# Performance work log

Hardware: AMD Instinct MI355X
Metric: run time of the kernel (lower is better)

Reference implementation:

```python
import jax, jax.numpy as jnp
import numpy as np

N = 50000   # nodes
E = 800000  # edges (before self-loops)
IN = 256    # in_dim
H = 4       # heads
C = 64      # out_dim per head
NEG_SLOPE = 0.2
BN_EPS = 1e-5


def setup_inputs() -> dict:
    key = jax.random.key(0)
    ks = jax.random.split(key, 6)
    feature = jax.random.normal(ks[0], (N, IN), jnp.float32)
    edge_index = jax.random.randint(ks[1], (2, E), 0, N, dtype=jnp.int64)
    W = jax.random.normal(ks[2], (IN, H * C), jnp.float32) * 0.05
    att_src = jax.random.normal(ks[3], (H, C), jnp.float32) * 0.1
    att_dst = jax.random.normal(ks[4], (H, C), jnp.float32) * 0.1
    bias = jnp.zeros((H * C,), jnp.float32)
    gamma = jnp.ones((H * C,), jnp.float32)
    beta = jnp.zeros((H * C,), jnp.float32)
    return {"feature": feature, "edge_index": edge_index, "W": W,
            "att_src": att_src, "att_dst": att_dst, "bias": bias,
            "gamma": gamma, "beta": beta}


def reference(feature, edge_index, W, att_src, att_dst, bias, gamma, beta):
    n = feature.shape[0]
    # linear projection -> [N, H, C]
    x = (feature @ W).reshape(n, H, C)
    # per-node attention logits [N, H]
    a_src = jnp.einsum('nhc,hc->nh', x, att_src)
    a_dst = jnp.einsum('nhc,hc->nh', x, att_dst)
    # add self loops (PyG GATConv default)
    loop = jnp.arange(n, dtype=edge_index.dtype)
    src = jnp.concatenate([edge_index[0], loop])
    dst = jnp.concatenate([edge_index[1], loop])
    # edge attention scores [E+N, H]
    e = jax.nn.leaky_relu(a_src[src] + a_dst[dst], NEG_SLOPE)
    # segment softmax over incoming edges of each dst node
    m = jax.ops.segment_max(e, dst, num_segments=n)
    ex = jnp.exp(e - m[dst])
    denom = jax.ops.segment_sum(ex, dst, num_segments=n)
    alpha = ex / denom[dst]                       # [E+N, H]
    # weighted message aggregation -> [N, H, C]
    msg = x[src] * alpha[:, :, None]
    out = jax.ops.segment_sum(msg, dst, num_segments=n)
    h = out.reshape(n, H * C) + bias
    # batchnorm over nodes (training-mode batch statistics)
    mu = jnp.mean(h, axis=0)
    var = jnp.var(h, axis=0)
    h = (h - mu) * jax.lax.rsqrt(var + BN_EPS) * gamma + beta
    # ELU activation
    h = jax.nn.elu(h)
    # residual (in_dim == out_dim * num_heads)
    return feature + h
```

## Files before the change

kernel.cpp:

```cpp
#include <hip/hip_runtime.h>

#define N_NODES 50000
#define N_EDGES 800000
#define NEG_SLOPE 0.2f
#define BN_EPS  1e-5f
#define LOG2E   1.44269504088896f

#define CHUNKS 256
#define EDGES_PER_CHUNK 3125
#define NCOARSE 1024
#define NBUCKET 782

typedef short bf16x8 __attribute__((ext_vector_type(8)));
typedef float floatx4 __attribute__((ext_vector_type(4)));

__device__ inline ushort f2bf(float f) {
    union { float f; unsigned u; } v; v.f = f;
    unsigned r = v.u + 0x7fff + ((v.u >> 16) & 1);
    return (ushort)(r >> 16);
}
__device__ inline float bf2f(ushort h) {
    union { unsigned u; float f; } v; v.u = ((unsigned)h) << 16;
    return v.f;
}

__global__ __launch_bounds__(256) void count_wt_kernel(const int* __restrict__ ei,
                                                       const float* __restrict__ W,
                                                       int* __restrict__ counts,
                                                       ushort* __restrict__ Wtb,
                                                       float* __restrict__ gsum,
                                                       float* __restrict__ gsumsq)
{
    __shared__ int hist[NCOARSE];
    const int t = threadIdx.x;
    const int b = blockIdx.x;
    if (b < CHUNKS) {
        for (int j = t; j < NCOARSE; j += 256) hist[j] = 0;
        __syncthreads();
        const int e0 = b * EDGES_PER_CHUNK;
        for (int e = e0 + t; e < e0 + EDGES_PER_CHUNK; e += 256)
            atomicAdd(&hist[ei[N_EDGES + e] >> 6], 1);
        __syncthreads();
        for (int j = t; j < NCOARSE; j += 256)
            counts[j * CHUNKS + b] = hist[j];
    } else {
        const int n = b - CHUNKS;
        Wtb[n * 256 + t] = f2bf(W[t * 256 + n]);
        if (n == 0) { gsum[t] = 0.f; gsumsq[t] = 0.f; }
    }
}

__global__ __launch_bounds__(256) void sscan1_kernel(int* __restrict__ counts,
                                                     int* __restrict__ blocksum)
{
    __shared__ int sm[256];
    const int t = threadIdx.x;
    const int i = blockIdx.x * 256 + t;
    const int v = counts[i];
    sm[t] = v;
    __syncthreads();
#pragma unroll
    for (int off = 1; off < 256; off <<= 1) {
        const int u = (t >= off) ? sm[t - off] : 0;
        __syncthreads();
        sm[t] += u;
        __syncthreads();
    }
    counts[i] = sm[t] - v;
    if (t == 255) blocksum[blockIdx.x] = sm[255];
}

__global__ __launch_bounds__(256) void bucket_scatter_kernel(const int* __restrict__ ei,
                                                             const int* __restrict__ counts,
                                                             const int* __restrict__ blocksum,
                                                             int* __restrict__ blockbase,
                                                             uint* __restrict__ tmp)
{
    __shared__ int sm[256];
    __shared__ int bbase[NCOARSE];
    __shared__ int cursor[NCOARSE];
    const int t = threadIdx.x;
    const int blk = blockIdx.x;

    int v[4], loc[4], tot = 0;
#pragma unroll
    for (int j = 0; j < 4; ++j) {
        v[j] = blocksum[t * 4 + j];
        loc[j] = tot;
        tot += v[j];
    }
    sm[t] = tot;
    __syncthreads();
#pragma unroll
    for (int off = 1; off < 256; off <<= 1) {
        const int u = (t >= off) ? sm[t - off] : 0;
        __syncthreads();
        sm[t] += u;
        __syncthreads();
    }
    const int base = sm[t] - tot;
#pragma unroll
    for (int j = 0; j < 4; ++j) bbase[t * 4 + j] = base + loc[j];
    if (blk == 0) {
#pragma unroll
        for (int j = 0; j < 4; ++j) blockbase[t * 4 + j] = base + loc[j];
    }
    __syncthreads();

    for (int u = t; u < NCOARSE; u += 256)
        cursor[u] = counts[u * CHUNKS + blk] + bbase[u];
    __syncthreads();
    const int e0 = blk * EDGES_PER_CHUNK;
    for (int e = e0 + t; e < e0 + EDGES_PER_CHUNK; e += 256) {
        const int src = ei[e];
        const int dst = ei[N_EDGES + e];
        const int pos = atomicAdd(&cursor[dst >> 6], 1);
        tmp[pos] = ((uint)src << 6) | (uint)(dst & 63);
    }
}

__global__ __launch_bounds__(256) void bucket_build_kernel(const uint* __restrict__ tmp,
                                                           const int* __restrict__ blockbase,
                                                           int* __restrict__ offsets,
                                                           int* __restrict__ csr_src)
{
    __shared__ int hist[64];
    __shared__ int sbuf[64];
    __shared__ int cursor[64];
    const int t = threadIdx.x;
    const int b = blockIdx.x;
    const int start = blockbase[b];
    const int end   = blockbase[b + 1];
    if (t < 64) hist[t] = 0;
    __syncthreads();
    for (int e = start + t; e < end; e += 256)
        atomicAdd(&hist[tmp[e] & 63], 1);
    __syncthreads();
    const int v = (t < 64) ? hist[t] : 0;
    if (t < 64) sbuf[t] = v;
    __syncthreads();
#pragma unroll
    for (int off = 1; off < 64; off <<= 1) {
        int u = 0;
        if (t < 64 && t >= off) u = sbuf[t - off];
        __syncthreads();
        if (t < 64) sbuf[t] += u;
        __syncthreads();
    }
    if (t < 64) {
        const int excl = start + sbuf[t] - v;
        cursor[t] = excl;
        const int node = b * 64 + t;
        if (node < N_NODES) offsets[node] = excl;
    }
    if (b == 0 && t == 0) offsets[N_NODES] = N_EDGES;
    __syncthreads();
    for (int e = start + t; e < end; e += 256) {
        const uint p = tmp[e];
        const int pos = atomicAdd(&cursor[p & 63], 1);
        csr_src[pos] = (int)(p >> 6);
    }
}

#define LDSTRIDE 40
__global__ __launch_bounds__(256) void gemm_kernel(const float* __restrict__ A,
                                                   const ushort* __restrict__ Bt,
                                                   const float* __restrict__ att_src,
                                                   const float* __restrict__ att_dst,
                                                   ushort* __restrict__ Xb,
                                                   float* __restrict__ s,
                                                   float* __restrict__ d)
{
    __shared__ ushort As[64 * LDSTRIDE];
    __shared__ ushort Bs[256 * LDSTRIDE];
    const int tid = threadIdx.x;
    const int lane = tid & 63;
    const int wid = tid >> 6;
    const int row0 = blockIdx.x * 64;
    const int quad = lane >> 4;
    const int l16  = lane & 15;

    floatx4 acc[4][4] = {};

    const int lr = tid >> 2;
    const int lk = (tid & 3) * 8;

    for (int k0 = 0; k0 < 256; k0 += 32) {
        {
            const int grow = row0 + lr;
            union { ushort u[8]; ulonglong2 v; } cv;
            if (grow < N_NODES) {
                const float4 f0 = *(const float4*)(A + (size_t)grow * 256 + k0 + lk);
                const float4 f1 = *(const float4*)(A + (size_t)grow * 256 + k0 + lk + 4);
                cv.u[0] = f2bf(f0.x); cv.u[1] = f2bf(f0.y);
                cv.u[2] = f2bf(f0.z); cv.u[3] = f2bf(f0.w);
                cv.u[4] = f2bf(f1.x); cv.u[5] = f2bf(f1.y);
                cv.u[6] = f2bf(f1.z); cv.u[7] = f2bf(f1.w);
            } else {
                cv.v = ulonglong2{0ull, 0ull};
            }
            *(ulonglong2*)(As + lr * LDSTRIDE + lk) = cv.v;
        }
#pragma unroll
        for (int r = 0; r < 4; ++r) {
            const int row = lr + r * 64;
            const ulonglong2 bv = *(const ulonglong2*)(Bt + (size_t)row * 256 + k0 + lk);
            *(ulonglong2*)(Bs + row * LDSTRIDE + lk) = bv;
        }
        __syncthreads();
        bf16x8 afrag[4], bfrag[4];
#pragma unroll
        for (int mi = 0; mi < 4; ++mi)
            afrag[mi] = *(const bf16x8*)(As + (mi * 16 + l16) * LDSTRIDE + quad * 8);
#pragma unroll
        for (int ni = 0; ni < 4; ++ni)
            bfrag[ni] = *(const bf16x8*)(Bs + (wid * 64 + ni * 16 + l16) * LDSTRIDE + quad * 8);
#pragma unroll
        for (int mi = 0; mi < 4; ++mi)
#pragma unroll
            for (int ni = 0; ni < 4; ++ni)
                acc[mi][ni] = __builtin_amdgcn_mfma_f32_16x16x32_bf16(afrag[mi], bfrag[ni], acc[mi][ni], 0, 0, 0);
        __syncthreads();
    }

    const int head = wid;
    float as_l[4], ad_l[4];
#pragma unroll
    for (int ni = 0; ni < 4; ++ni) {
        const int ch = head * 64 + ni * 16 + l16;
        as_l[ni] = att_src[ch];
        ad_l[ni] = att_dst[ch];
    }
#pragma unroll
    for (int mi = 0; mi < 4; ++mi) {
#pragma unroll
        for (int r = 0; r < 4; ++r) {
            const int grow = row0 + mi * 16 + quad * 4 + r;
            const bool ok = grow < N_NODES;
            float vs = 0.f, vd = 0.f;
            ushort4 o;
#pragma unroll
            for (int ni = 0; ni < 4; ++ni) {
                const float v = acc[mi][ni][r];
                vs += v * as_l[ni];
                vd += v * ad_l[ni];
                ((ushort*)&o)[ni] = f2bf(v);
            }
            if (ok)
                *(ushort4*)(Xb + (size_t)grow * 256 + head * 64 + l16 * 4) = o;
#pragma unroll
            for (int m = 8; m >= 1; m >>= 1) {
                vs += __shfl_xor(vs, m);
                vd += __shfl_xor(vd, m);
            }
            if (l16 == 0 && ok) {
                s[grow * 4 + head] = vs * LOG2E;
                d[grow * 4 + head] = vd * LOG2E;
            }
        }
    }
}

__global__ __launch_bounds__(256) void aggregate_kernel(const ushort* __restrict__ xb,
                                                        const float* __restrict__ s,
                                                        const float* __restrict__ d,
                                                        const int* __restrict__ offsets,
                                                        const int* __restrict__ csr_src,
                                                        ushort* __restrict__ hagg)
{
    const int wid = threadIdx.x >> 6;
    const int lane = threadIdx.x & 63;
    const int n = blockIdx.x * 4 + wid;
    if (n >= N_NODES) return;
    const int h = lane >> 4;
    const float dn = d[n * 4 + h];
    const float sn = s[n * 4 + h];
    const ushort4 xr = *(const ushort4*)(xb + (size_t)n * 256 + lane * 4);
    float eself = sn + dn;
    eself = eself >= 0.f ? eself : NEG_SLOPE * eself;
    const float pself = exp2f(eself);
    float den = pself;
    float a0 = pself * bf2f(xr.x), a1 = pself * bf2f(xr.y);
    float a2 = pself * bf2f(xr.z), a3 = pself * bf2f(xr.w);
    const int e0 = __builtin_amdgcn_readfirstlane(offsets[n]);
    const int e1 = __builtin_amdgcn_readfirstlane(offsets[n + 1]);
    int e = e0;
    for (; e + 8 <= e1; e += 8) {
        int si[8];
        float lg[8];
        ushort4 xv[8];
#pragma unroll
        for (int j = 0; j < 8; ++j) si[j] = __builtin_amdgcn_readfirstlane(csr_src[e + j]);
#pragma unroll
        for (int j = 0; j < 8; ++j) lg[j] = s[si[j] * 4 + h] + dn;
#pragma unroll
        for (int j = 0; j < 8; ++j)
            xv[j] = *(const ushort4*)(xb + (size_t)si[j] * 256 + lane * 4);
#pragma unroll
        for (int j = 0; j < 8; ++j) {
            float l = lg[j];
            l = l >= 0.f ? l : NEG_SLOPE * l;
            const float p = exp2f(l);
            den += p;
            a0 += p * bf2f(xv[j].x);
            a1 += p * bf2f(xv[j].y);
            a2 += p * bf2f(xv[j].z);
            a3 += p * bf2f(xv[j].w);
        }
    }
    for (; e < e1; ++e) {
        const int src = __builtin_amdgcn_readfirstlane(csr_src[e]);
        float ee = s[src * 4 + h] + dn;
        ee = ee >= 0.f ? ee : NEG_SLOPE * ee;
        const float pe = exp2f(ee);
        const ushort4 xs = *(const ushort4*)(xb + (size_t)src * 256 + lane * 4);
        a0 += pe * bf2f(xs.x); a1 += pe * bf2f(xs.y);
        a2 += pe * bf2f(xs.z); a3 += pe * bf2f(xs.w);
        den += pe;
    }
    const float inv = 1.0f / den;
    ushort4 o;
    o.x = f2bf(a0 * inv); o.y = f2bf(a1 * inv);
    o.z = f2bf(a2 * inv); o.w = f2bf(a3 * inv);
    *(ushort4*)(hagg + (size_t)n * 256 + lane * 4) = o;
}

#define BN_BLOCKS 784
__global__ __launch_bounds__(256) void bn_stats_kernel(const ushort* __restrict__ hagg,
                                                       float* __restrict__ gsum,
                                                       float* __restrict__ gsumsq)
{
    const int c = threadIdx.x;
    const int r0 = blockIdx.x * 64;
    float sum = 0.f, sq = 0.f;
#pragma unroll 4
    for (int i = 0; i < 64; ++i) {
        const int r = r0 + i;
        if (r < N_NODES) {
            const float v = bf2f(hagg[(size_t)r * 256 + c]);
            sum += v;
            sq += v * v;
        }
    }
    atomicAdd(&gsum[c], sum);
    atomicAdd(&gsumsq[c], sq);
}

__global__ __launch_bounds__(256) void finalize_kernel(const float* __restrict__ feature,
                                                       const ushort* __restrict__ hagg,
                                                       const float* __restrict__ gsum,
                                                       const float* __restrict__ gsumsq,
                                                       const float* __restrict__ gamma,
                                                       const float* __restrict__ beta,
                                                       float* __restrict__ out)
{
    __shared__ ushort hs[16][264];
    const int t = threadIdx.x;
    const int wid = t >> 6;
    const int lane = t & 63;
    const int row0 = blockIdx.x * 16;
    const int hblk = lane >> 4;
    const int l16 = lane & 15;

#pragma unroll
    for (int rr = 0; rr < 4; ++rr) {
        const int r = wid * 4 + rr;
        const int n = row0 + r;
        const ushort4 hv = *(const ushort4*)(hagg + (size_t)n * 256 + lane * 4);
        hs[r][hblk * 64 + 0 * 16 + l16] = hv.x;
        hs[r][hblk * 64 + 1 * 16 + l16] = hv.y;
        hs[r][hblk * 64 + 2 * 16 + l16] = hv.z;
        hs[r][hblk * 64 + 3 * 16 + l16] = hv.w;
    }

    float meanv[4], scalev[4], betav[4];
#pragma unroll
    for (int j = 0; j < 4; ++j) {
        const int tc = lane * 4 + j;
        const int w = tc & 63;
        const int p = (tc >> 6) * 64 + ((w & 15) << 2) + (w >> 4);
        const float m = gsum[p] * (1.0f / N_NODES);
        const float var = gsumsq[p] * (1.0f / N_NODES) - m * m;
        meanv[j] = m;
        scalev[j] = gamma[tc] * rsqrtf(var + BN_EPS);
        betav[j] = beta[tc];
    }
    __syncthreads();

#pragma unroll
    for (int rr = 0; rr < 4; ++rr) {
        const int r = wid * 4 + rr;
        const int n = row0 + r;
        const ushort4 hv = *(const ushort4*)(&hs[r][lane * 4]);
        const float4 fv = *(const float4*)(feature + (size_t)n * 256 + lane * 4);
        const float hvf[4] = {bf2f(hv.x), bf2f(hv.y), bf2f(hv.z), bf2f(hv.w)};
        float4 o;
        float* op = (float*)&o;
        const float* fp = (const float*)&fv;
#pragma unroll
        for (int j = 0; j < 4; ++j) {
            float v = (hvf[j] - meanv[j]) * scalev[j] + betav[j];
            v = v > 0.f ? v : expm1f(v);
            op[j] = v + fp[j];
        }
        *(float4*)(out + (size_t)n * 256 + lane * 4) = o;
    }
}

extern "C" void kernel_launch(void* const* d_in, const int* in_sizes, int n_in,
                              void* d_out, int out_size, void* d_ws, size_t ws_size,
                              hipStream_t stream)
{
    const float* feature = (const float*)d_in[0];
    const int*   ei      = (const int*)d_in[1];
    const float* W       = (const float*)d_in[2];
    const float* att_src = (const float*)d_in[3];
    const float* att_dst = (const float*)d_in[4];
    const float* gamma   = (const float*)d_in[6];
    const float* beta    = (const float*)d_in[7];
    float* out = (float*)d_out;

    char* w = (char*)d_ws;
    auto carve = [&](size_t bytes) {
        char* p = w;
        w += (bytes + 255) & ~(size_t)255;
        return p;
    };
    ushort* Wtb      = (ushort*)carve((size_t)256 * 256 * 2);
    ushort* xb       = (ushort*)carve((size_t)N_NODES * 256 * 2);
    ushort* hagg     = (ushort*)carve((size_t)N_NODES * 256 * 2);
    float*  s        = (float*)carve((size_t)N_NODES * 4 * 4);
    float*  dv       = (float*)carve((size_t)N_NODES * 4 * 4);
    int*    counts   = (int*)carve((size_t)NCOARSE * CHUNKS * 4);
    int*    offsets  = (int*)carve((size_t)(N_NODES + 1) * 4);
    int*    csr_src  = (int*)carve((size_t)N_EDGES * 4);
    int*    blocksum = (int*)carve((size_t)NCOARSE * 4);
    int*    blockbase= (int*)carve((size_t)NCOARSE * 4);
    float*  gsum     = (float*)carve(256 * 4);
    float*  gsumsq   = (float*)carve(256 * 4);
    uint*   tmp      = (uint*)hagg;

    count_wt_kernel<<<512, 256, 0, stream>>>(ei, W, counts, Wtb, gsum, gsumsq);
    sscan1_kernel<<<NCOARSE, 256, 0, stream>>>(counts, blocksum);
    bucket_scatter_kernel<<<CHUNKS, 256, 0, stream>>>(ei, counts, blocksum, blockbase, tmp);
    bucket_build_kernel<<<NBUCKET, 256, 0, stream>>>(tmp, blockbase, offsets, csr_src);
    gemm_kernel<<<782, 256, 0, stream>>>(feature, Wtb, att_src, att_dst, xb, s, dv);
    aggregate_kernel<<<12500, 256, 0, stream>>>(xb, s, dv, offsets, csr_src, hagg);
    bn_stats_kernel<<<BN_BLOCKS, 256, 0, stream>>>(hagg, gsum, gsumsq);
    finalize_kernel<<<3125, 256, 0, stream>>>(feature, hagg, gsum, gsumsq, gamma, beta, out);
}
```

Measured before the change: 274.9 us.

## Fuse bucket scatter with GEMM and BN stats into aggregation

Merges the edge bucket-scatter kernel and the projection GEMM into one launch with block-range dispatch, so the two independent stages run concurrently. Batchnorm statistics are now accumulated inside the aggregation kernel through per-block shared reductions and atomics spread over 8 replicas, which removes a separate pass over hagg. The aggregation tail loop is folded into the unrolled 8-wide loop using masked logits, and the finalize kernel remaps blocks and stages the BN parameters in shared memory. The cost is more global atomics from 12500 blocks and extra shared memory plus syncs in aggregation.

After: 243.4 us. 1.13x faster.

```diff
diff --git a/kernel.cpp b/kernel.cpp
--- a/kernel.cpp
+++ b/kernel.cpp
@@ -10,6 +10,7 @@
 #define EDGES_PER_CHUNK 3125
 #define NCOARSE 1024
 #define NBUCKET 782
+#define GEMM_BLOCKS 782
 
 typedef short bf16x8 __attribute__((ext_vector_type(8)));
 typedef float floatx4 __attribute__((ext_vector_type(4)));
@@ -28,8 +29,7 @@
                                                        const float* __restrict__ W,
                                                        int* __restrict__ counts,
                                                        ushort* __restrict__ Wtb,
-                                                       float* __restrict__ gsum,
-                                                       float* __restrict__ gsumsq)
+                                                       float* __restrict__ bnacc)
 {
     __shared__ int hist[NCOARSE];
     const int t = threadIdx.x;
@@ -46,7 +46,7 @@
     } else {
         const int n = b - CHUNKS;
         Wtb[n * 256 + t] = f2bf(W[t * 256 + n]);
-        if (n == 0) { gsum[t] = 0.f; gsumsq[t] = 0.f; }
+        if (n < 16) bnacc[n * 256 + t] = 0.f;
     }
 }
 
@@ -70,113 +70,73 @@
     if (t == 255) blocksum[blockIdx.x] = sm[255];
 }
 
-__global__ __launch_bounds__(256) void bucket_scatter_kernel(const int* __restrict__ ei,
-                                                             const int* __restrict__ counts,
-                                                             const int* __restrict__ blocksum,
-                                                             int* __restrict__ blockbase,
-                                                             uint* __restrict__ tmp)
-{
-    __shared__ int sm[256];
-    __shared__ int bbase[NCOARSE];
-    __shared__ int cursor[NCOARSE];
-    const int t = threadIdx.x;
-    const int blk = blockIdx.x;
-
-    int v[4], loc[4], tot = 0;
-#pragma unroll
-    for (int j = 0; j < 4; ++j) {
-        v[j] = blocksum[t * 4 + j];
-        loc[j] = tot;
-        tot += v[j];
-    }
-    sm[t] = tot;
-    __syncthreads();
-#pragma unroll
-    for (int off = 1; off < 256; off <<= 1) {
-        const int u = (t >= off) ? sm[t - off] : 0;
-        __syncthreads();
-        sm[t] += u;
-        __syncthreads();
-    }
-    const int base = sm[t] - tot;
-#pragma unroll
-    for (int j = 0; j < 4; ++j) bbase[t * 4 + j] = base + loc[j];
-    if (blk == 0) {
-#pragma unroll
-        for (int j = 0; j < 4; ++j) blockbase[t * 4 + j] = base + loc[j];
-    }
-    __syncthreads();
-
-    for (int u = t; u < NCOARSE; u += 256)
-        cursor[u] = counts[u * CHUNKS + blk] + bbase[u];
-    __syncthreads();
-    const int e0 = blk * EDGES_PER_CHUNK;
-    for (int e = e0 + t; e < e0 + EDGES_PER_CHUNK; e += 256) {
-        const int src = ei[e];
-        const int dst = ei[N_EDGES + e];
-        const int pos = atomicAdd(&cursor[dst >> 6], 1);
-        tmp[pos] = ((uint)src << 6) | (uint)(dst & 63);
-    }
-}
-
-__global__ __launch_bounds__(256) void bucket_build_kernel(const uint* __restrict__ tmp,
-                                                           const int* __restrict__ blockbase,
-                                                           int* __restrict__ offsets,
-                                                           int* __restrict__ csr_src)
-{
-    __shared__ int hist[64];
-    __shared__ int sbuf[64];
-    __shared__ int cursor[64];
-    const int t = threadIdx.x;
-    const int b = blockIdx.x;
-    const int start = blockbase[b];
-    const int end   = blockbase[b + 1];
-    if (t < 64) hist[t] = 0;
-    __syncthreads();
-    for (int e = start + t; e < end; e += 256)
-        atomicAdd(&hist[tmp[e] & 63], 1);
-    __syncthreads();
-    const int v = (t < 64) ? hist[t] : 0;
-    if (t < 64) sbuf[t] = v;
-    __syncthreads();
-#pragma unroll
-    for (int off = 1; off < 64; off <<= 1) {
-        int u = 0;
-        if (t < 64 && t >= off) u = sbuf[t - off];
-        __syncthreads();
-        if (t < 64) sbuf[t] += u;
-        __syncthreads();
-    }
-    if (t < 64) {
-        const int excl = start + sbuf[t] - v;
-        cursor[t] = excl;
-        const int node = b * 64 + t;
-        if (node < N_NODES) offsets[node] = excl;
-    }
-    if (b == 0 && t == 0) offsets[N_NODES] = N_EDGES;
-    __syncthreads();
-    for (int e = start + t; e < end; e += 256) {
-        const uint p = tmp[e];
-        const int pos = atomicAdd(&cursor[p & 63], 1);
-        csr_src[pos] = (int)(p >> 6);
-    }
-}
-
 #define LDSTRIDE 40
-__global__ __launch_bounds__(256) void gemm_kernel(const float* __restrict__ A,
-                                                   const ushort* __restrict__ Bt,
-                                                   const float* __restrict__ att_src,
-                                                   const float* __restrict__ att_dst,
-                                                   ushort* __restrict__ Xb,
-                                                   float* __restrict__ s,
-                                                   float* __restrict__ d)
-{
-    __shared__ ushort As[64 * LDSTRIDE];
-    __shared__ ushort Bs[256 * LDSTRIDE];
+__global__ __launch_bounds__(256) void scatter_gemm_kernel(const int* __restrict__ ei,
+                                                           const int* __restrict__ counts,
+                                                           const int* __restrict__ blocksum,
+                                                           int* __restrict__ blockbase,
+                                                           uint* __restrict__ tmp,
+                                                           const float* __restrict__ A,
+                                                           const ushort* __restrict__ Bt,
+                                                           const float* __restrict__ att_src,
+                                                           const float* __restrict__ att_dst,
+                                                           ushort* __restrict__ Xb,
+                                                           float* __restrict__ s,
+                                                           float* __restrict__ d)
+{
+    __shared__ __align__(16) char smem[25600];
     const int tid = threadIdx.x;
+
+    if (blockIdx.x < CHUNKS) {
+        int* sm     = (int*)smem;
+        int* bbase  = sm + 256;
+        int* cursor = bbase + NCOARSE;
+        const int t = tid;
+        const int blk = blockIdx.x;
+
+        int v[4], loc[4], tot = 0;
+#pragma unroll
+        for (int j = 0; j < 4; ++j) {
+            v[j] = blocksum[t * 4 + j];
+            loc[j] = tot;
+            tot += v[j];
+        }
+        sm[t] = tot;
+        __syncthreads();
+#pragma unroll
+        for (int off = 1; off < 256; off <<= 1) {
+            const int u = (t >= off) ? sm[t - off] : 0;
+            __syncthreads();
+            sm[t] += u;
+            __syncthreads();
+        }
+        const int base = sm[t] - tot;
+#pragma unroll
+        for (int j = 0; j < 4; ++j) bbase[t * 4 + j] = base + loc[j];
+        if (blk == 0) {
+#pragma unroll
+            for (int j = 0; j < 4; ++j) blockbase[t * 4 + j] = base + loc[j];
+        }
+        __syncthreads();
+
+        for (int u = t; u < NCOARSE; u += 256)
+            cursor[u] = counts[u * CHUNKS + blk] + bbase[u];
+        __syncthreads();
+        const int e0 = blk * EDGES_PER_CHUNK;
+        for (int e = e0 + t; e < e0 + EDGES_PER_CHUNK; e += 256) {
+            const int src = ei[e];
+            const int dst = ei[N_EDGES + e];
+            const int pos = atomicAdd(&cursor[dst >> 6], 1);
+            tmp[pos] = ((uint)src << 6) | (uint)(dst & 63);
+        }
+        return;
+    }
+
+    ushort* As = (ushort*)smem;
+    ushort* Bs = As + 64 * LDSTRIDE;
     const int lane = tid & 63;
     const int wid = tid >> 6;
-    const int row0 = blockIdx.x * 64;
+    const int row0 = (blockIdx.x - CHUNKS) * 64;
     const int quad = lane >> 4;
     const int l16  = lane & 15;
 
@@ -261,17 +221,62 @@
     }
 }
 
+__global__ __launch_bounds__(256) void bucket_build_kernel(const uint* __restrict__ tmp,
+                                                           const int* __restrict__ blockbase,
+                                                           int* __restrict__ offsets,
+                                                           int* __restrict__ csr_src)
+{
+    __shared__ int hist[64];
+    __shared__ int sbuf[64];
+    __shared__ int cursor[64];
+    const int t = threadIdx.x;
+    const int b = blockIdx.x;
+    const int start = blockbase[b];
+    const int end   = blockbase[b + 1];
+    if (t < 64) hist[t] = 0;
+    __syncthreads();
+    for (int e = start + t; e < end; e += 256)
+        atomicAdd(&hist[tmp[e] & 63], 1);
+    __syncthreads();
+    const int v = (t < 64) ? hist[t] : 0;
+    if (t < 64) sbuf[t] = v;
+    __syncthreads();
+#pragma unroll
+    for (int off = 1; off < 64; off <<= 1) {
+        int u = 0;
+        if (t < 64 && t >= off) u = sbuf[t - off];
+        __syncthreads();
+        if (t < 64) sbuf[t] += u;
+        __syncthreads();
+    }
+    if (t < 64) {
+        const int excl = start + sbuf[t] - v;
+        cursor[t] = excl;
+        const int node = b * 64 + t;
+        if (node < N_NODES) offsets[node] = excl;
+    }
+    if (b == 0 && t == 0) offsets[N_NODES] = N_EDGES;
+    __syncthreads();
+    for (int e = start + t; e < end; e += 256) {
+        const uint p = tmp[e];
+        const int pos = atomicAdd(&cursor[p & 63], 1);
+        csr_src[pos] = (int)(p >> 6);
+    }
+}
+
 __global__ __launch_bounds__(256) void aggregate_kernel(const ushort* __restrict__ xb,
                                                         const float* __restrict__ s,
                                                         const float* __restrict__ d,
                                                         const int* __restrict__ offsets,
                                                         const int* __restrict__ csr_src,
-                                                        ushort* __restrict__ hagg)
-{
+                                                        ushort* __restrict__ hagg,
+                                                        float* __restrict__ bnacc)
+{
+    __shared__ float bsum[4][256];
+    __shared__ float bsq[4][256];
     const int wid = threadIdx.x >> 6;
     const int lane = threadIdx.x & 63;
     const int n = blockIdx.x * 4 + wid;
-    if (n >= N_NODES) return;
     const int h = lane >> 4;
     const float dn = d[n * 4 + h];
     const float sn = s[n * 4 + h];
@@ -284,13 +289,16 @@
     float a2 = pself * bf2f(xr.z), a3 = pself * bf2f(xr.w);
     const int e0 = __builtin_amdgcn_readfirstlane(offsets[n]);
     const int e1 = __builtin_amdgcn_readfirstlane(offsets[n + 1]);
-    int e = e0;
-    for (; e + 8 <= e1; e += 8) {
+    for (int e = e0; e < e1; e += 8) {
         int si[8];
         float lg[8];
         ushort4 xv[8];
 #pragma unroll
-        for (int j = 0; j < 8; ++j) si[j] = __builtin_amdgcn_readfirstlane(csr_src[e + j]);
+        for (int j = 0; j < 8; ++j) {
+            const int idx = e + j;
+            const int idx2 = idx < e1 ? idx : e1 - 1;
+            si[j] = __builtin_amdgcn_readfirstlane(csr_src[idx2]);
+        }
 #pragma unroll
         for (int j = 0; j < 8; ++j) lg[j] = s[si[j] * 4 + h] + dn;
 #pragma unroll
@@ -298,7 +306,7 @@
             xv[j] = *(const ushort4*)(xb + (size_t)si[j] * 256 + lane * 4);
 #pragma unroll
         for (int j = 0; j < 8; ++j) {
-            float l = lg[j];
+            float l = (e + j < e1) ? lg[j] : -1e30f;
             l = l >= 0.f ? l : NEG_SLOPE * l;
             const float p = exp2f(l);
             den += p;
@@ -308,102 +316,93 @@
             a3 += p * bf2f(xv[j].w);
         }
     }
-    for (; e < e1; ++e) {
-        const int src = __builtin_amdgcn_readfirstlane(csr_src[e]);
-        float ee = s[src * 4 + h] + dn;
-        ee = ee >= 0.f ? ee : NEG_SLOPE * ee;
-        const float pe = exp2f(ee);
-        const ushort4 xs = *(const ushort4*)(xb + (size_t)src * 256 + lane * 4);
-        a0 += pe * bf2f(xs.x); a1 += pe * bf2f(xs.y);
-        a2 += pe * bf2f(xs.z); a3 += pe * bf2f(xs.w);
-        den += pe;
-    }
     const float inv = 1.0f / den;
     ushort4 o;
     o.x = f2bf(a0 * inv); o.y = f2bf(a1 * inv);
     o.z = f2bf(a2 * inv); o.w = f2bf(a3 * inv);
     *(ushort4*)(hagg + (size_t)n * 256 + lane * 4) = o;
-}
-
-#define BN_BLOCKS 784
-__global__ __launch_bounds__(256) void bn_stats_kernel(const ushort* __restrict__ hagg,
-                                                       float* __restrict__ gsum,
-                                                       float* __restrict__ gsumsq)
-{
+
+    const float v0 = bf2f(o.x), v1 = bf2f(o.y), v2 = bf2f(o.z), v3 = bf2f(o.w);
+    *(float4*)&bsum[wid][lane * 4] = float4{v0, v1, v2, v3};
+    *(float4*)&bsq[wid][lane * 4]  = float4{v0 * v0, v1 * v1, v2 * v2, v3 * v3};
+    __syncthreads();
     const int c = threadIdx.x;
-    const int r0 = blockIdx.x * 64;
-    float sum = 0.f, sq = 0.f;
-#pragma unroll 4
-    for (int i = 0; i < 64; ++i) {
-        const int r = r0 + i;
-        if (r < N_NODES) {
-            const float v = bf2f(hagg[(size_t)r * 256 + c]);
-            sum += v;
-            sq += v * v;
-        }
-    }
-    atomicAdd(&gsum[c], sum);
-    atomicAdd(&gsumsq[c], sq);
+    const float smv = bsum[0][c] + bsum[1][c] + bsum[2][c] + bsum[3][c];
+    const float sqv = bsq[0][c]  + bsq[1][c]  + bsq[2][c]  + bsq[3][c];
+    const int rep = (blockIdx.x & 7) * 256 + c;
+    atomicAdd(&bnacc[rep], smv);
+    atomicAdd(&bnacc[2048 + rep], sqv);
 }
 
 __global__ __launch_bounds__(256) void finalize_kernel(const float* __restrict__ feature,
                                                        const ushort* __restrict__ hagg,
-                                                       const float* __restrict__ gsum,
-                                                       const float* __restrict__ gsumsq,
+                                                       const float* __restrict__ bnacc,
                                                        const float* __restrict__ gamma,
                                                        const float* __restrict__ beta,
                                                        float* __restrict__ out)
 {
     __shared__ ushort hs[16][264];
+    __shared__ float meanS[256], scaleS[256], betaS[256];
     const int t = threadIdx.x;
     const int wid = t >> 6;
     const int lane = t & 63;
-    const int row0 = blockIdx.x * 16;
+    const int x = blockIdx.x & 7;
+    const int i = blockIdx.x >> 3;
+    const int bk = (i * 4 + wid) * 8 + x;
+    const bool active = bk < 12500;
     const int hblk = lane >> 4;
     const int l16 = lane & 15;
 
-#pragma unroll
-    for (int rr = 0; rr < 4; ++rr) {
-        const int r = wid * 4 + rr;
-        const int n = row0 + r;
-        const ushort4 hv = *(const ushort4*)(hagg + (size_t)n * 256 + lane * 4);
-        hs[r][hblk * 64 + 0 * 16 + l16] = hv.x;
-        hs[r][hblk * 64 + 1 * 16 + l16] = hv.y;
-        hs[r][hblk * 64 + 2 * 16 + l16] = hv.z;
-        hs[r][hblk * 64 + 3 * 16 + l16] = hv.w;
-    }
-
-    float meanv[4], scalev[4], betav[4];
-#pragma unroll
-    for (int j = 0; j < 4; ++j) {
-        const int tc = lane * 4 + j;
-        const int w = tc & 63;
-        const int p = (tc >> 6) * 64 + ((w & 15) << 2) + (w >> 4);
-        const float m = gsum[p] * (1.0f / N_NODES);
-        const float var = gsumsq[p] * (1.0f / N_NODES) - m * m;
-        meanv[j] = m;
-        scalev[j] = gamma[tc] * rsqrtf(var + BN_EPS);
-        betav[j] = beta[tc];
-    }
-    __syncthreads();
-
-#pragma unroll
-    for (int rr = 0; rr < 4; ++rr) {
-        const int r = wid * 4 + rr;
-        const int n = row0 + r;
-        const ushort4 hv = *(const ushort4*)(&hs[r][lane * 4]);
-        const float4 fv = *(const float4*)(feature + (size_t)n * 256 + lane * 4);
-        const float hvf[4] = {bf2f(hv.x), bf2f(hv.y), bf2f(hv.z), bf2f(hv.w)};
-        float4 o;
-        float* op = (float*)&o;
-        const float* fp = (const float*)&fv;
-#pragma unroll
-        for (int j = 0; j < 4; ++j) {
-            float v = (hvf[j] - meanv[j]) * scalev[j] + betav[j];
-            v = v > 0.f ? v : expm1f(v);
-            op[j] = v + fp[j];
-        }
-        *(float4*)(out + (size_t)n * 256 + lane * 4) = o;
+    if (active) {
+#pragma unroll
+        for (int rr = 0; rr < 4; ++rr) {
+            const int r = wid * 4 + rr;
+            const int n = bk * 4 + rr;
+            const ushort4 hv = *(const ushort4*)(hagg + (size_t)n * 256 + lane * 4);
+            hs[r][hblk * 64 + 0 * 16 + l16] = hv.x;
+            hs[r][hblk * 64 + 1 * 16 + l16] = hv.y;
+            hs[r][hblk * 64 + 2 * 16 + l16] = hv.z;
+            hs[r][hblk * 64 + 3 * 16 + l16] = hv.w;
+        }
+    }
+
+    {
+        float smv = 0.f, sqv = 0.f;
+#pragma unroll
+        for (int r = 0; r < 8; ++r) {
+            smv += bnacc[r * 256 + t];
+            sqv += bnacc[2048 + r * 256 + t];
+        }
+        const float m = smv * (1.0f / N_NODES);
+        const float var = sqv * (1.0f / N_NODES) - m * m;
+        const int w = t & 63;
+        const int tc = (t >> 6) * 64 + (w & 3) * 16 + (w >> 2);
+        meanS[tc] = m;
+        scaleS[tc] = gamma[tc] * rsqrtf(var + BN_EPS);
+        betaS[tc] = beta[tc];
+    }
+    __syncthreads();
+
+    if (active) {
+#pragma unroll
+        for (int rr = 0; rr < 4; ++rr) {
+            const int r = wid * 4 + rr;
+            const int n = bk * 4 + rr;
+            const ushort4 hv = *(const ushort4*)(&hs[r][lane * 4]);
+            const float4 fv = *(const float4*)(feature + (size_t)n * 256 + lane * 4);
+            const float hvf[4] = {bf2f(hv.x), bf2f(hv.y), bf2f(hv.z), bf2f(hv.w)};
+            float4 o;
+            float* op = (float*)&o;
+            const float* fp = (const float*)&fv;
+#pragma unroll
+            for (int j = 0; j < 4; ++j) {
+                const int ch = lane * 4 + j;
+                float v = (hvf[j] - meanS[ch]) * scaleS[ch] + betaS[ch];
+                v = v > 0.f ? v : expm1f(v);
+                op[j] = v + fp[j];
+            }
+            *(float4*)(out + (size_t)n * 256 + lane * 4) = o;
+        }
     }
 }
 
@@ -436,16 +435,15 @@
     int*    csr_src  = (int*)carve((size_t)N_EDGES * 4);
     int*    blocksum = (int*)carve((size_t)NCOARSE * 4);
     int*    blockbase= (int*)carve((size_t)NCOARSE * 4);
-    float*  gsum     = (float*)carve(256 * 4);
-    float*  gsumsq   = (float*)carve(256 * 4);
+    float*  bnacc    = (float*)carve((size_t)4096 * 4);
     uint*   tmp      = (uint*)hagg;
 
-    count_wt_kernel<<<512, 256, 0, stream>>>(ei, W, counts, Wtb, gsum, gsumsq);
+    count_wt_kernel<<<512, 256, 0, stream>>>(ei, W, counts, Wtb, bnacc);
     sscan1_kernel<<<NCOARSE, 256, 0, stream>>>(counts, blocksum);
-    bucket_scatter_kernel<<<CHUNKS, 256, 0, stream>>>(ei, counts, blocksum, blockbase, tmp);
+    scatter_gemm_kernel<<<CHUNKS + GEMM_BLOCKS, 256, 0, stream>>>(
+        ei, counts, blocksum, blockbase, tmp,
+        feature, Wtb, att_src, att_dst, xb, s, dv);
     bucket_build_kernel<<<NBUCKET, 256, 0, stream>>>(tmp, blockbase, offsets, csr_src);
-    gemm_kernel<<<782, 256, 0, stream>>>(feature, Wtb, att_src, att_dst, xb, s, dv);
-    aggregate_kernel<<<12500, 256, 0, stream>>>(xb, s, dv, offsets, csr_src, hagg);
-    bn_stats_kernel<<<BN_BLOCKS, 256, 0, stream>>>(hagg, gsum, gsumsq);
-    finalize_kernel<<<3125, 256, 0, stream>>>(feature, hagg, gsum, gsumsq, gamma, beta, out);
-}
+    aggregate_kernel<<<12500, 256, 0, stream>>>(xb, s, dv, offsets, csr_src, hagg, bnacc);
+    finalize_kernel<<<3136, 256, 0, stream>>>(feature, hagg, bnacc, gamma, beta, out);
+}
```
